# Optimization experiments

Measured on AMD Instinct MI355X. Metric: run time of the kernel, lower is better.

## Reference

```python
import jax, jax.numpy as jnp
import numpy as np

G = 1024      # graphs per batch
NPG = 64      # nodes per graph
M = 512       # undirected edges per graph (stored both directions)
N = G * NPG   # 65536 nodes
E = G * 2 * M # 1048576 directed edges
F_IN = 128
HID = 128
CLS = 10
RATIO = 0.5   # top-k edge ratio (forward arg `ratio`); eval phase (train_phase=False)


def setup_inputs() -> dict:
    rng = np.random.default_rng(0)
    # random undirected edges within each graph, i < j guaranteed
    a = rng.integers(0, NPG, (G, M))
    b = rng.integers(0, NPG - 1, (G, M))
    b = b + (b >= a)  # b != a
    i = np.minimum(a, b)
    j = np.maximum(a, b)
    off = (np.arange(G) * NPG)[:, None]
    src = (np.concatenate([i, j], axis=1) + off).reshape(-1).astype(np.int32)
    dst = (np.concatenate([j, i], axis=1) + off).reshape(-1).astype(np.int32)
    # reverse-edge pairing: within each graph block of 2M edges, fwd e <-> e+M
    rev = (np.concatenate([np.arange(M) + M, np.arange(M)])[None, :]
           + (np.arange(G) * 2 * M)[:, None]).reshape(-1).astype(np.int32)
    batch = np.repeat(np.arange(G), NPG).astype(np.int32)

    key = jax.random.key(0)
    ks = jax.random.split(key, 8)

    def lin(k, fi, fo):
        return jax.random.normal(k, (fi, fo), jnp.float32) / np.sqrt(fi).astype(np.float32)

    return dict(
        x=jax.random.normal(ks[0], (N, F_IN), jnp.float32),
        src=jnp.asarray(src), dst=jnp.asarray(dst), rev=jnp.asarray(rev),
        batch=jnp.asarray(batch),
        W0=lin(ks[1], F_IN, HID), b0=jnp.zeros((HID,), jnp.float32),
        W1=lin(ks[2], HID, HID), b1=jnp.zeros((HID,), jnp.float32),
        W2=lin(ks[3], HID, HID), b2=jnp.zeros((HID,), jnp.float32),
        lw1=lin(ks[4], HID, HID), lb1=jnp.zeros((HID,), jnp.float32),
        lw2=lin(ks[5], HID, CLS), lb2=jnp.zeros((CLS,), jnp.float32),
    )


def gcn_conv(x, W, b, src, dst, ew):
    # PyG GCNConv with self-loops (fill 1) and symmetric normalization
    h = x @ W                                      # [N,H]
    deg = jax.ops.segment_sum(ew, dst, num_segments=N) + 1.0
    dinv = jax.lax.rsqrt(deg)                      # deg >= 1 (relu'd x => ew >= 0)
    norm = dinv[src] * ew * dinv[dst]              # [E]
    agg = jax.ops.segment_sum(norm[:, None] * h[src], dst, num_segments=N)
    return agg + (dinv * dinv)[:, None] * h + b    # self-loop term + bias


def reference(x, src, dst, rev, batch, W0, b0, W1, b1, W2, b2, lw1, lb1, lw2, lb2):
    ones_e = jnp.ones((E,), x.dtype)
    x1 = jax.nn.relu(gcn_conv(x, W0, b0, src, dst, ones_e))

    # edge scores on relu'd features (nonnegative)
    scores = jnp.sum(x1[src] * x1[dst], axis=-1)   # [E]
    gid = batch[src]                               # per-edge graph id (nondecreasing)
    mask = src < dst                               # one direction per undirected edge

    # per-graph (segment) top-k over masked edges: rank within segment by score desc
    smask = jnp.where(mask, scores, -jnp.inf)
    perm = jnp.lexsort((-smask, gid))              # primary: gid, secondary: score desc
    counts = jax.ops.segment_sum(jnp.ones((E,), jnp.int32), gid, num_segments=G)
    start = jnp.cumsum(counts) - counts            # exclusive segment starts
    rank = jnp.zeros((E,), jnp.int32).at[perm].set(
        jnp.arange(E, dtype=jnp.int32) - start[gid[perm]])
    m = jax.ops.segment_sum(mask.astype(jnp.int32), gid, num_segments=G)
    k = jnp.ceil(RATIO * m.astype(jnp.float32)).astype(jnp.int32)
    sel = mask & (rank < k[gid])
    sampled = (sel | sel[rev]).astype(x.dtype)     # mirror to reverse direction

    ew = scores * sampled                          # sparse edge weights
    x2 = jax.nn.relu(gcn_conv(x1, W1, b1, src, dst, ew))
    x3 = jax.nn.relu(gcn_conv(x2, W2, b2, src, dst, ew))

    # global mean pool over nodes per graph
    nc = jax.ops.segment_sum(jnp.ones((N,), x.dtype), batch, num_segments=G)
    pooled = jax.ops.segment_sum(x3, batch, num_segments=G) / nc[:, None]

    h = jax.nn.relu(pooled @ lw1 + lb1)            # dropout is identity at eval
    logits = h @ lw2 + lb2
    return (jax.nn.log_softmax(logits, axis=-1), sampled, counts)
```

## Files before the change

kernel.cpp:

```cpp
#include <hip/hip_runtime.h>

#define G_   1024
#define NPG_ 64
#define EPG_ 1024
#define MPG_ 512
#define F_   128
#define E_   (G_*EPG_)

typedef __attribute__((ext_vector_type(8))) short bf16x8;
typedef __attribute__((ext_vector_type(4))) float f32x4;

__device__ __forceinline__ unsigned short f2bf(float f) {
    union { float f; unsigned int u; } v; v.f = f;
    unsigned int r = v.u + 0x7fffu + ((v.u >> 16) & 1u);
    return (unsigned short)(r >> 16);
}
__device__ __forceinline__ unsigned int packbf(float a, float b) {
    return (unsigned int)f2bf(a) | ((unsigned int)f2bf(b) << 16);
}

#define XASW(r, cb) ((((r) << 4) + ((cb) ^ ((r) & 15))) << 3)
#define AFSW(r, b)  ((((r) << 3) + ((b) ^ ((r) & 7))) << 3)

__global__ __launch_bounds__(256) void k_pack_w(const float* __restrict__ W0,
    const float* __restrict__ W1, const float* __restrict__ W2,
    unsigned short* __restrict__ Wp)
{
    int idx = blockIdx.x * 256 + threadIdx.x;
    int wsel = idx >> 11;
    int r = idx & 2047;
    int lane = r & 63, tc = (r >> 6) & 7, kb = r >> 9;
    const float* W = (wsel == 0) ? W0 : ((wsel == 1) ? W1 : W2);
    int col  = tc * 16 + (lane & 15);
    int row0 = kb * 32 + (lane >> 4) * 8;
    unsigned int p0 = packbf(W[(row0+0)*F_+col], W[(row0+1)*F_+col]);
    unsigned int p1 = packbf(W[(row0+2)*F_+col], W[(row0+3)*F_+col]);
    unsigned int p2 = packbf(W[(row0+4)*F_+col], W[(row0+5)*F_+col]);
    unsigned int p3 = packbf(W[(row0+6)*F_+col], W[(row0+7)*F_+col]);
    *(uint4*)(Wp + (size_t)wsel * 16384 + (size_t)r * 8) = make_uint4(p0,p1,p2,p3);
}

__global__ __launch_bounds__(256, 4) void k_fused(
    const float* __restrict__ x, const int* __restrict__ src, const int* __restrict__ dst,
    const unsigned short* __restrict__ Wp,
    const float* __restrict__ b0, const float* __restrict__ b1, const float* __restrict__ b2,
    const float* __restrict__ lw1, const float* __restrict__ lb1,
    const float* __restrict__ lw2, const float* __restrict__ lb2,
    float* __restrict__ out_log, float* __restrict__ out_sampled,
    float* __restrict__ out_counts)
{
    const int g = blockIdx.x, t = threadIdx.x;
    const int l = t & 63, w = t >> 6;
    const int q = l >> 4, cl = l & 15;
    const int base_e = g * EPG_, base_n = g * NPG_;

    __shared__ alignas(16) unsigned short XA[8192];
    __shared__ alignas(16) float buf1[4224];
    __shared__ alignas(16) float sc[MPG_];
    __shared__ unsigned char sl[EPG_], dl[EPG_];
    __shared__ int hist_i[256];
    __shared__ unsigned long long mlist[96];
    __shared__ int wsum[4];
    __shared__ float redzf[8];
    __shared__ int ideg[NPG_];
    __shared__ float dinv[NPG_];
    __shared__ int mcnt, bstar, Rrem;

    float* mtmp = (float*)hist_i;
    unsigned int*   a1p = (unsigned int*)buf1;
    unsigned short* af1 = (unsigned short*)buf1 + 4224;
    unsigned short* af2 = (unsigned short*)buf1;

    const float4* xsrc = (const float4*)(x + (size_t)base_n * F_);
    for (int i = t; i < 2048; i += 256) {
        int v = i >> 5, c4 = i & 31;
        float4 xv = xsrc[i];
        int si = XASW(v, c4 >> 1) + (c4 & 1) * 4;
        unsigned int* d2 = (unsigned int*)&XA[si];
        d2[0] = packbf(xv.x, xv.y);
        d2[1] = packbf(xv.z, xv.w);
    }
    for (int i = t; i < 2112; i += 256) a1p[i] = 0u;
    if (t < NPG_) ideg[t] = 0;
    __syncthreads();

    for (int e = t; e < EPG_; e += 256) {
        int s = src[base_e + e] - base_n;
        int d = dst[base_e + e] - base_n;
        sl[e] = (unsigned char)s; dl[e] = (unsigned char)d;
        atomicAdd(&ideg[d], 1);
        atomicAdd(&a1p[d * 33 + (s >> 1)], 1u << ((s & 1) * 16));
    }
    __syncthreads();
    if (t < NPG_) dinv[t] = rsqrtf((float)(ideg[t] + 1));
    __syncthreads();
    for (int i = t; i < 4096; i += 256) {
        int v = i >> 6, s = i & 63;
        unsigned int m = (a1p[v * 33 + (s >> 1)] >> ((s & 1) * 16)) & 0xFFFFu;
        float a = dinv[v] * dinv[s] * (float)m;
        if (v == s) a += dinv[v] * dinv[v];
        af1[AFSW(v, s >> 3) + (s & 7)] = f2bf(a);
    }
    __syncthreads();

    auto conv = [&](const unsigned short* WpX, const unsigned short* AFp,
                    const float* bias, int writeXA) {
        f32x4 cA[4][2];
        #pragma unroll
        for (int rb = 0; rb < 4; rb++) { cA[rb][0] = (f32x4)0.0f; cA[rb][1] = (f32x4)0.0f; }
        #pragma unroll
        for (int kb = 0; kb < 4; kb++) {
            bf16x8 a[4];
            #pragma unroll
            for (int rb = 0; rb < 4; rb++)
                a[rb] = *(const bf16x8*)&XA[XASW(rb*16 + cl, kb*4 + q)];
            #pragma unroll
            for (int tcw = 0; tcw < 2; tcw++) {
                int tc = 2*w + tcw;
                bf16x8 b = *(const bf16x8*)&WpX[((kb*8 + tc)*64 + l)*8];
                #pragma unroll
                for (int rb = 0; rb < 4; rb++)
                    cA[rb][tcw] = __builtin_amdgcn_mfma_f32_16x16x32_bf16(
                                      a[rb], b, cA[rb][tcw], 0, 0, 0);
            }
        }
        __syncthreads();
        #pragma unroll
        for (int rb = 0; rb < 4; rb++)
            #pragma unroll
            for (int tcw = 0; tcw < 2; tcw++) {
                int tc = 2*w + tcw;
                #pragma unroll
                for (int rp = 0; rp < 2; rp++) {
                    int r0 = rb*16 + q*4 + rp*2;
                    int idx = ((r0 >> 5)*8 + tc)*512 + (((r0 >> 3) & 3)*16 + cl)*8 + (r0 & 7);
                    *(unsigned int*)&XA[idx] = packbf(cA[rb][tcw][rp*2], cA[rb][tcw][rp*2+1]);
                }
            }
        __syncthreads();
        f32x4 cB[4][2];
        #pragma unroll
        for (int rb = 0; rb < 4; rb++) { cB[rb][0] = (f32x4)0.0f; cB[rb][1] = (f32x4)0.0f; }
        #pragma unroll
        for (int kb2 = 0; kb2 < 2; kb2++) {
            bf16x8 a2[4];
            #pragma unroll
            for (int rb = 0; rb < 4; rb++)
                a2[rb] = *(const bf16x8*)&AFp[AFSW(rb*16 + cl, kb2*4 + q)];
            #pragma unroll
            for (int tcw = 0; tcw < 2; tcw++) {
                int tc = 2*w + tcw;
                bf16x8 b2 = *(const bf16x8*)&XA[((kb2*8 + tc)*64 + l)*8];
                #pragma unroll
                for (int rb = 0; rb < 4; rb++)
                    cB[rb][tcw] = __builtin_amdgcn_mfma_f32_16x16x32_bf16(
                                      a2[rb], b2, cB[rb][tcw], 0, 0, 0);
            }
        }
        __syncthreads();
        #pragma unroll
        for (int tcw = 0; tcw < 2; tcw++) {
            int colb = (2*w + tcw)*16 + cl;
            float bv = bias[colb];
            if (writeXA) {
                #pragma unroll
                for (int rb = 0; rb < 4; rb++)
                    #pragma unroll
                    for (int reg = 0; reg < 4; reg++) {
                        int row = rb*16 + q*4 + reg;
                        XA[XASW(row, colb >> 3) + (colb & 7)] =
                            f2bf(fmaxf(cB[rb][tcw][reg] + bv, 0.0f));
                    }
            } else {
                float ps = 0.0f;
                #pragma unroll
                for (int rb = 0; rb < 4; rb++)
                    #pragma unroll
                    for (int reg = 0; reg < 4; reg++)
                        ps += fmaxf(cB[rb][tcw][reg] + bv, 0.0f);
                atomicAdd(&sc[colb], ps);
            }
        }
    };

    conv(Wp, af1, b0, 1);
    __syncthreads();

    {
        f32x4 cg[4];
        #pragma unroll
        for (int tcg = 0; tcg < 4; tcg++) cg[tcg] = (f32x4)0.0f;
        #pragma unroll
        for (int kb = 0; kb < 4; kb++) {
            bf16x8 a = *(const bf16x8*)&XA[XASW(w*16 + cl, kb*4 + q)];
            #pragma unroll
            for (int tcg = 0; tcg < 4; tcg++) {
                bf16x8 b = *(const bf16x8*)&XA[XASW(tcg*16 + cl, kb*4 + q)];
                cg[tcg] = __builtin_amdgcn_mfma_f32_16x16x32_bf16(a, b, cg[tcg], 0, 0, 0);
            }
        }
        #pragma unroll
        for (int tcg = 0; tcg < 4; tcg++)
            #pragma unroll
            for (int reg = 0; reg < 4; reg++)
                buf1[(w*16 + q*4 + reg)*66 + tcg*16 + cl] = cg[tcg][reg];
    }
    __syncthreads();

    float sA, sB;
    {
        sA = buf1[(int)sl[t]*66 + dl[t]];
        sB = buf1[(int)sl[t+256]*66 + dl[t+256]];
        sc[t] = sA; sc[t + 256] = sB;
    }
    if (t < NPG_) dinv[t] = 1.0f;
    __syncthreads();

    int selA, selB;
    {
        float mn = fminf(sA, sB), mx = fmaxf(sA, sB);
        #pragma unroll
        for (int off = 32; off >= 1; off >>= 1) {
            mn = fminf(mn, __shfl_xor(mn, off, 64));
            mx = fmaxf(mx, __shfl_xor(mx, off, 64));
        }
        if (l == 0) { redzf[w] = mn; redzf[4 + w] = mx; }
        hist_i[t] = 0;
        if (t == 0) mcnt = 0;
        __syncthreads();
        mn = fminf(fminf(redzf[0], redzf[1]), fminf(redzf[2], redzf[3]));
        mx = fmaxf(fmaxf(redzf[4], redzf[5]), fmaxf(redzf[6], redzf[7]));
        float scale = 255.0f / fmaxf(mx - mn, 1e-20f);
        int binA = (int)fminf((sA - mn) * scale, 255.0f);
        int binB = (int)fminf((sB - mn) * scale, 255.0f);
        atomicAdd(&hist_i[binA], 1);
        atomicAdd(&hist_i[binB], 1);
        __syncthreads();
        int h = hist_i[t];
        int v = h;
        #pragma unroll
        for (int off = 1; off < 64; off <<= 1) {
            int n = __shfl_down(v, off, 64);
            if (l + off < 64) v += n;
        }
        if (l == 0) wsum[w] = v;
        __syncthreads();
        int suf = v;
        for (int w2 = w + 1; w2 < 4; w2++) suf += wsum[w2];
        int cgt = suf - h;
        if (suf >= 256 && cgt < 256) { bstar = t; Rrem = 256 - cgt; }
        __syncthreads();
        const int bs = bstar, Rr = Rrem;
        unsigned long long keyA = ((unsigned long long)__float_as_uint(sA) << 32)
                                | (unsigned int)(0xFFFFFFFFu - (unsigned)t);
        unsigned long long keyB = ((unsigned long long)__float_as_uint(sB) << 32)
                                | (unsigned int)(0xFFFFFFFFu - (unsigned)(t + 256));
        if (binA == bs) { int p = atomicAdd(&mcnt, 1); if (p < 96) mlist[p] = keyA; }
        if (binB == bs) { int p = atomicAdd(&mcnt, 1); if (p < 96) mlist[p] = keyB; }
        __syncthreads();
        const int mc = mcnt;
        auto sel_edge = [&](float s, int e, int bin, unsigned long long key) -> int {
            if (bin > bs) return 1;
            if (bin < bs) return 0;
            if (mc <= 96) {
                int r = 0;
                for (int j2 = 0; j2 < mc; j2++) r += (mlist[j2] > key) ? 1 : 0;
                return r < Rr;
            }
            int r = 0;
            for (int ep = 0; ep < MPG_; ep++) {
                float sp = sc[ep];
                r += (sp > s || (sp == s && ep < e)) ? 1 : 0;
            }
            return r < 256;
        };
        selA = sel_edge(sA, t, binA, keyA);
        selB = sel_edge(sB, t + 256, binB, keyB);
        float sfA = selA ? 1.0f : 0.0f, sfB = selB ? 1.0f : 0.0f;
        out_sampled[base_e + t] = sfA;
        out_sampled[base_e + MPG_ + t] = sfA;
        out_sampled[base_e + t + 256] = sfB;
        out_sampled[base_e + MPG_ + t + 256] = sfB;
    }
    for (int i = t; i < 4224; i += 256) buf1[i] = 0.0f;
    __syncthreads();
    if (selA) {
        atomicAdd(&dinv[dl[t]], sA); atomicAdd(&dinv[sl[t]], sA);
        atomicAdd(&buf1[(int)dl[t]*66 + sl[t]], sA);
        atomicAdd(&buf1[(int)sl[t]*66 + dl[t]], sA);
    }
    if (selB) {
        atomicAdd(&dinv[dl[t+256]], sB); atomicAdd(&dinv[sl[t+256]], sB);
        atomicAdd(&buf1[(int)dl[t+256]*66 + sl[t+256]], sB);
        atomicAdd(&buf1[(int)sl[t+256]*66 + dl[t+256]], sB);
    }
    __syncthreads();
    if (t < NPG_) dinv[t] = rsqrtf(dinv[t]);
    __syncthreads();
    {
        float st[4];
        #pragma unroll
        for (int k2 = 0; k2 < 4; k2++) {
            int i = k2*256 + t; int vv = i >> 6, ss = i & 63;
            float a = dinv[vv] * dinv[ss] * buf1[vv*66 + ss];
            if (vv == ss) a += dinv[vv] * dinv[vv];
            st[k2] = a;
        }
        __syncthreads();
        #pragma unroll
        for (int k2 = 0; k2 < 4; k2++) {
            int i = k2*256 + t; int vv = i >> 6, ss = i & 63;
            af2[AFSW(vv, ss >> 3) + (ss & 7)] = f2bf(st[k2]);
        }
        for (int i = 1024 + t; i < 4096; i += 256) {
            int vv = i >> 6, ss = i & 63;
            float a = dinv[vv] * dinv[ss] * buf1[vv*66 + ss];
            if (vv == ss) a += dinv[vv] * dinv[vv];
            af2[AFSW(vv, ss >> 3) + (ss & 7)] = f2bf(a);
        }
    }
    __syncthreads();

    conv(Wp + 16384, af2, b1, 1);
    __syncthreads();

    if (t < F_) sc[t] = 0.0f;
    conv(Wp + 32768, af2, b2, 0);
    __syncthreads();

    {
        int c = t & 127, hh = t >> 7;
        float p = 0.0f;
        for (int kk = 0; kk < 64; kk++) {
            int k2 = hh*64 + kk;
            p = fmaf(sc[k2], lw1[(size_t)k2 * F_ + c], p);
        }
        mtmp[t] = p;
    }
    __syncthreads();
    if (t >= 128 && t < 138) buf1[200 + (t - 128)] = 0.0f;
    if (t < F_)
        buf1[t] = fmaxf(lb1[t] + (mtmp[t] + mtmp[t + 128]) * (1.0f/64.0f), 0.0f);
    __syncthreads();
    if (t < 160) {
        int o = t >> 4, seg = t & 15;
        float p = 0.0f;
        #pragma unroll
        for (int kk = 0; kk < 8; kk++) {
            int k2 = seg*8 + kk;
            p = fmaf(buf1[k2], lw2[(size_t)k2 * 10 + o], p);
        }
        atomicAdd(&buf1[200 + o], p);
    }
    __syncthreads();
    if (t < 10) {
        float lg = buf1[200 + t] + lb2[t];
        float m = -1e30f;
        #pragma unroll
        for (int q2 = 0; q2 < 10; q2++) m = fmaxf(m, buf1[200 + q2] + lb2[q2]);
        float se = 0.0f;
        #pragma unroll
        for (int q2 = 0; q2 < 10; q2++) se += expf(buf1[200 + q2] + lb2[q2] - m);
        out_log[(size_t)g * 10 + t] = lg - m - logf(se);
    }
    if (t == 0) out_counts[g] = 1024.0f;
}

extern "C" void kernel_launch(void* const* d_in, const int* in_sizes, int n_in,
                              void* d_out, int out_size, void* d_ws, size_t ws_size,
                              hipStream_t stream) {
    const float* x    = (const float*)d_in[0];
    const int*   src  = (const int*)  d_in[1];
    const int*   dst  = (const int*)  d_in[2];
    const float* W0   = (const float*)d_in[5];
    const float* b0   = (const float*)d_in[6];
    const float* W1   = (const float*)d_in[7];
    const float* b1   = (const float*)d_in[8];
    const float* W2   = (const float*)d_in[9];
    const float* b2   = (const float*)d_in[10];
    const float* lw1  = (const float*)d_in[11];
    const float* lb1  = (const float*)d_in[12];
    const float* lw2  = (const float*)d_in[13];
    const float* lb2  = (const float*)d_in[14];

    float* out_log     = (float*)d_out;
    float* out_sampled = out_log + (size_t)G_ * 10;
    float* out_counts  = out_sampled + (size_t)E_;

    unsigned short* Wp = (unsigned short*)d_ws;

    k_pack_w<<<24, 256, 0, stream>>>(W0, W1, W2, Wp);
    k_fused<<<G_, 256, 0, stream>>>(x, src, dst, Wp, b0, b1, b2,
                                    lw1, lb1, lw2, lb2,
                                    out_log, out_sampled, out_counts);
}
```

Baseline: 48.45 us.

## Preload weights into registers and overlap conv stages with graph preprocessing

Splits the conv lambda into separate stages. Weight fragments are now loaded into registers ahead of use, and the first X·W MFMA overlaps construction of the normalized adjacency. The second layer's X·W GEMM is fused into the gram-score MFMA loop because it reads the same activations, and several barriers are removed by moving the buffer clears and the sc reset earlier. Edge loading is also vectorised to int4 per thread. The cost is higher register pressure (three sets of eight bf16x8 weight fragments plus accumulators), which could lower occupancy or cause spills.

```diff
diff --git a/kernel.cpp b/kernel.cpp
--- a/kernel.cpp
+++ b/kernel.cpp
@@ -71,6 +71,81 @@
     unsigned short* af1 = (unsigned short*)buf1 + 4224;
     unsigned short* af2 = (unsigned short*)buf1;
 
+    auto loadW = [&](const unsigned short* WpX, bf16x8 (&wr)[8]) {
+        #pragma unroll
+        for (int kb = 0; kb < 4; kb++)
+            #pragma unroll
+            for (int tcw = 0; tcw < 2; tcw++)
+                wr[kb*2+tcw] = *(const bf16x8*)&WpX[((kb*8 + 2*w+tcw)*64 + l)*8];
+    };
+    auto mfma_step1 = [&](const bf16x8 (&wr)[8], f32x4 (&cX)[4][2]) {
+        #pragma unroll
+        for (int rb = 0; rb < 4; rb++) { cX[rb][0] = (f32x4)0.0f; cX[rb][1] = (f32x4)0.0f; }
+        #pragma unroll
+        for (int kb = 0; kb < 4; kb++) {
+            bf16x8 a[4];
+            #pragma unroll
+            for (int rb = 0; rb < 4; rb++)
+                a[rb] = *(const bf16x8*)&XA[XASW(rb*16 + cl, kb*4 + q)];
+            #pragma unroll
+            for (int tcw = 0; tcw < 2; tcw++)
+                #pragma unroll
+                for (int rb = 0; rb < 4; rb++)
+                    cX[rb][tcw] = __builtin_amdgcn_mfma_f32_16x16x32_bf16(
+                                      a[rb], wr[kb*2+tcw], cX[rb][tcw], 0, 0, 0);
+        }
+    };
+    auto write_xw = [&](const f32x4 (&cX)[4][2]) {
+        #pragma unroll
+        for (int rb = 0; rb < 4; rb++)
+            #pragma unroll
+            for (int tcw = 0; tcw < 2; tcw++) {
+                int tc = 2*w + tcw;
+                #pragma unroll
+                for (int rp = 0; rp < 2; rp++) {
+                    int r0 = rb*16 + q*4 + rp*2;
+                    int idx = ((r0 >> 5)*8 + tc)*512 + (((r0 >> 3) & 3)*16 + cl)*8 + (r0 & 7);
+                    *(unsigned int*)&XA[idx] = packbf(cX[rb][tcw][rp*2], cX[rb][tcw][rp*2+1]);
+                }
+            }
+    };
+    auto mfma_step2 = [&](const unsigned short* AFp, f32x4 (&cX)[4][2]) {
+        #pragma unroll
+        for (int rb = 0; rb < 4; rb++) { cX[rb][0] = (f32x4)0.0f; cX[rb][1] = (f32x4)0.0f; }
+        #pragma unroll
+        for (int kb2 = 0; kb2 < 2; kb2++) {
+            bf16x8 a2[4];
+            #pragma unroll
+            for (int rb = 0; rb < 4; rb++)
+                a2[rb] = *(const bf16x8*)&AFp[AFSW(rb*16 + cl, kb2*4 + q)];
+            #pragma unroll
+            for (int tcw = 0; tcw < 2; tcw++) {
+                bf16x8 b2 = *(const bf16x8*)&XA[((kb2*8 + 2*w+tcw)*64 + l)*8];
+                #pragma unroll
+                for (int rb = 0; rb < 4; rb++)
+                    cX[rb][tcw] = __builtin_amdgcn_mfma_f32_16x16x32_bf16(
+                                      a2[rb], b2, cX[rb][tcw], 0, 0, 0);
+            }
+        }
+    };
+    auto epilogue_H = [&](const f32x4 (&cX)[4][2], const float* bias) {
+        #pragma unroll
+        for (int tcw = 0; tcw < 2; tcw++) {
+            int colb = (2*w + tcw)*16 + cl;
+            float bv = bias[colb];
+            #pragma unroll
+            for (int rb = 0; rb < 4; rb++)
+                #pragma unroll
+                for (int reg = 0; reg < 4; reg++) {
+                    int row = rb*16 + q*4 + reg;
+                    XA[XASW(row, colb >> 3) + (colb & 7)] =
+                        f2bf(fmaxf(cX[rb][tcw][reg] + bv, 0.0f));
+                }
+        }
+    };
+
+    bf16x8 wr1[8];
+    loadW(Wp, wr1);
     const float4* xsrc = (const float4*)(x + (size_t)base_n * F_);
     for (int i = t; i < 2048; i += 256) {
         int v = i >> 5, c4 = i & 31;
@@ -84,120 +159,74 @@
     if (t < NPG_) ideg[t] = 0;
     __syncthreads();
 
-    for (int e = t; e < EPG_; e += 256) {
-        int s = src[base_e + e] - base_n;
-        int d = dst[base_e + e] - base_n;
-        sl[e] = (unsigned char)s; dl[e] = (unsigned char)d;
-        atomicAdd(&ideg[d], 1);
-        atomicAdd(&a1p[d * 33 + (s >> 1)], 1u << ((s & 1) * 16));
+    {
+        int4 s4 = ((const int4*)(src + base_e))[t];
+        int4 d4 = ((const int4*)(dst + base_e))[t];
+        int s0 = s4.x - base_n, s1 = s4.y - base_n, s2 = s4.z - base_n, s3 = s4.w - base_n;
+        int d0 = d4.x - base_n, d1 = d4.y - base_n, d2 = d4.z - base_n, d3 = d4.w - base_n;
+        *(uchar4*)&sl[t*4] = make_uchar4((unsigned char)s0, (unsigned char)s1,
+                                         (unsigned char)s2, (unsigned char)s3);
+        *(uchar4*)&dl[t*4] = make_uchar4((unsigned char)d0, (unsigned char)d1,
+                                         (unsigned char)d2, (unsigned char)d3);
+        atomicAdd(&ideg[d0], 1); atomicAdd(&ideg[d1], 1);
+        atomicAdd(&ideg[d2], 1); atomicAdd(&ideg[d3], 1);
+        atomicAdd(&a1p[d0 * 33 + (s0 >> 1)], 1u << ((s0 & 1) * 16));
+        atomicAdd(&a1p[d1 * 33 + (s1 >> 1)], 1u << ((s1 & 1) * 16));
+        atomicAdd(&a1p[d2 * 33 + (s2 >> 1)], 1u << ((s2 & 1) * 16));
+        atomicAdd(&a1p[d3 * 33 + (s3 >> 1)], 1u << ((s3 & 1) * 16));
     }
     __syncthreads();
     if (t < NPG_) dinv[t] = rsqrtf((float)(ideg[t] + 1));
     __syncthreads();
-    for (int i = t; i < 4096; i += 256) {
-        int v = i >> 6, s = i & 63;
-        unsigned int m = (a1p[v * 33 + (s >> 1)] >> ((s & 1) * 16)) & 0xFFFFu;
-        float a = dinv[v] * dinv[s] * (float)m;
-        if (v == s) a += dinv[v] * dinv[v];
-        af1[AFSW(v, s >> 3) + (s & 7)] = f2bf(a);
-    }
-    __syncthreads();
-
-    auto conv = [&](const unsigned short* WpX, const unsigned short* AFp,
-                    const float* bias, int writeXA) {
+
+    {
         f32x4 cA[4][2];
-        #pragma unroll
-        for (int rb = 0; rb < 4; rb++) { cA[rb][0] = (f32x4)0.0f; cA[rb][1] = (f32x4)0.0f; }
+        mfma_step1(wr1, cA);
+        for (int i = t; i < 4096; i += 256) {
+            int v = i >> 6, s = i & 63;
+            unsigned int m = (a1p[v * 33 + (s >> 1)] >> ((s & 1) * 16)) & 0xFFFFu;
+            float a = dinv[v] * dinv[s] * (float)m;
+            if (v == s) a += dinv[v] * dinv[v];
+            af1[AFSW(v, s >> 3) + (s & 7)] = f2bf(a);
+        }
+        __syncthreads();
+        write_xw(cA);
+    }
+    __syncthreads();
+
+    bf16x8 wr2[8];
+    loadW(Wp + 16384, wr2);
+    {
+        f32x4 cB[4][2];
+        mfma_step2(af1, cB);
+        __syncthreads();
+        epilogue_H(cB, b0);
+    }
+    __syncthreads();
+
+    f32x4 cC[4][2];
+    {
+        f32x4 cg[4];
+        #pragma unroll
+        for (int tcg = 0; tcg < 4; tcg++) cg[tcg] = (f32x4)0.0f;
+        #pragma unroll
+        for (int rb = 0; rb < 4; rb++) { cC[rb][0] = (f32x4)0.0f; cC[rb][1] = (f32x4)0.0f; }
         #pragma unroll
         for (int kb = 0; kb < 4; kb++) {
-            bf16x8 a[4];
+            bf16x8 a_g = *(const bf16x8*)&XA[XASW(w*16 + cl, kb*4 + q)];
+            bf16x8 a2[4];
             #pragma unroll
             for (int rb = 0; rb < 4; rb++)
-                a[rb] = *(const bf16x8*)&XA[XASW(rb*16 + cl, kb*4 + q)];
-            #pragma unroll
-            for (int tcw = 0; tcw < 2; tcw++) {
-                int tc = 2*w + tcw;
-                bf16x8 b = *(const bf16x8*)&WpX[((kb*8 + tc)*64 + l)*8];
+                a2[rb] = *(const bf16x8*)&XA[XASW(rb*16 + cl, kb*4 + q)];
+            #pragma unroll
+            for (int tcg = 0; tcg < 4; tcg++)
+                cg[tcg] = __builtin_amdgcn_mfma_f32_16x16x32_bf16(a_g, a2[tcg], cg[tcg], 0, 0, 0);
+            #pragma unroll
+            for (int tcw = 0; tcw < 2; tcw++)
                 #pragma unroll
                 for (int rb = 0; rb < 4; rb++)
-                    cA[rb][tcw] = __builtin_amdgcn_mfma_f32_16x16x32_bf16(
-                                      a[rb], b, cA[rb][tcw], 0, 0, 0);
-            }
-        }
-        __syncthreads();
-        #pragma unroll
-        for (int rb = 0; rb < 4; rb++)
-            #pragma unroll
-            for (int tcw = 0; tcw < 2; tcw++) {
-                int tc = 2*w + tcw;
-                #pragma unroll
-                for (int rp = 0; rp < 2; rp++) {
-                    int r0 = rb*16 + q*4 + rp*2;
-                    int idx = ((r0 >> 5)*8 + tc)*512 + (((r0 >> 3) & 3)*16 + cl)*8 + (r0 & 7);
-                    *(unsigned int*)&XA[idx] = packbf(cA[rb][tcw][rp*2], cA[rb][tcw][rp*2+1]);
-                }
-            }
-        __syncthreads();
-        f32x4 cB[4][2];
-        #pragma unroll
-        for (int rb = 0; rb < 4; rb++) { cB[rb][0] = (f32x4)0.0f; cB[rb][1] = (f32x4)0.0f; }
-        #pragma unroll
-        for (int kb2 = 0; kb2 < 2; kb2++) {
-            bf16x8 a2[4];
-            #pragma unroll
-            for (int rb = 0; rb < 4; rb++)
-                a2[rb] = *(const bf16x8*)&AFp[AFSW(rb*16 + cl, kb2*4 + q)];
-            #pragma unroll
-            for (int tcw = 0; tcw < 2; tcw++) {
-                int tc = 2*w + tcw;
-                bf16x8 b2 = *(const bf16x8*)&XA[((kb2*8 + tc)*64 + l)*8];
-                #pragma unroll
-                for (int rb = 0; rb < 4; rb++)
-                    cB[rb][tcw] = __builtin_amdgcn_mfma_f32_16x16x32_bf16(
-                                      a2[rb], b2, cB[rb][tcw], 0, 0, 0);
-            }
-        }
-        __syncthreads();
-        #pragma unroll
-        for (int tcw = 0; tcw < 2; tcw++) {
-            int colb = (2*w + tcw)*16 + cl;
-            float bv = bias[colb];
-            if (writeXA) {
-                #pragma unroll
-                for (int rb = 0; rb < 4; rb++)
-                    #pragma unroll
-                    for (int reg = 0; reg < 4; reg++) {
-                        int row = rb*16 + q*4 + reg;
-                        XA[XASW(row, colb >> 3) + (colb & 7)] =
-                            f2bf(fmaxf(cB[rb][tcw][reg] + bv, 0.0f));
-                    }
-            } else {
-                float ps = 0.0f;
-                #pragma unroll
-                for (int rb = 0; rb < 4; rb++)
-                    #pragma unroll
-                    for (int reg = 0; reg < 4; reg++)
-                        ps += fmaxf(cB[rb][tcw][reg] + bv, 0.0f);
-                atomicAdd(&sc[colb], ps);
-            }
-        }
-    };
-
-    conv(Wp, af1, b0, 1);
-    __syncthreads();
-
-    {
-        f32x4 cg[4];
-        #pragma unroll
-        for (int tcg = 0; tcg < 4; tcg++) cg[tcg] = (f32x4)0.0f;
-        #pragma unroll
-        for (int kb = 0; kb < 4; kb++) {
-            bf16x8 a = *(const bf16x8*)&XA[XASW(w*16 + cl, kb*4 + q)];
-            #pragma unroll
-            for (int tcg = 0; tcg < 4; tcg++) {
-                bf16x8 b = *(const bf16x8*)&XA[XASW(tcg*16 + cl, kb*4 + q)];
-                cg[tcg] = __builtin_amdgcn_mfma_f32_16x16x32_bf16(a, b, cg[tcg], 0, 0, 0);
-            }
+                    cC[rb][tcw] = __builtin_amdgcn_mfma_f32_16x16x32_bf16(
+                                      a2[rb], wr2[kb*2+tcw], cC[rb][tcw], 0, 0, 0);
         }
         #pragma unroll
         for (int tcg = 0; tcg < 4; tcg++)
@@ -208,15 +237,11 @@
     __syncthreads();
 
     float sA, sB;
-    {
-        sA = buf1[(int)sl[t]*66 + dl[t]];
-        sB = buf1[(int)sl[t+256]*66 + dl[t+256]];
-        sc[t] = sA; sc[t + 256] = sB;
-    }
+    write_xw(cC);
+    sA = buf1[(int)sl[t]*66 + dl[t]];
+    sB = buf1[(int)sl[t+256]*66 + dl[t+256]];
+    sc[t] = sA; sc[t + 256] = sB;
     if (t < NPG_) dinv[t] = 1.0f;
-    __syncthreads();
-
-    int selA, selB;
     {
         float mn = fminf(sA, sB), mx = fmaxf(sA, sB);
         #pragma unroll
@@ -225,16 +250,21 @@
             mx = fmaxf(mx, __shfl_xor(mx, off, 64));
         }
         if (l == 0) { redzf[w] = mn; redzf[4 + w] = mx; }
-        hist_i[t] = 0;
-        if (t == 0) mcnt = 0;
-        __syncthreads();
-        mn = fminf(fminf(redzf[0], redzf[1]), fminf(redzf[2], redzf[3]));
-        mx = fmaxf(fmaxf(redzf[4], redzf[5]), fmaxf(redzf[6], redzf[7]));
+    }
+    hist_i[t] = 0;
+    if (t == 0) mcnt = 0;
+    __syncthreads();
+
+    int selA, selB;
+    {
+        float mn = fminf(fminf(redzf[0], redzf[1]), fminf(redzf[2], redzf[3]));
+        float mx = fmaxf(fmaxf(redzf[4], redzf[5]), fmaxf(redzf[6], redzf[7]));
         float scale = 255.0f / fmaxf(mx - mn, 1e-20f);
         int binA = (int)fminf((sA - mn) * scale, 255.0f);
         int binB = (int)fminf((sB - mn) * scale, 255.0f);
         atomicAdd(&hist_i[binA], 1);
         atomicAdd(&hist_i[binB], 1);
+        for (int i = t; i < 4224; i += 256) buf1[i] = 0.0f;
         __syncthreads();
         int h = hist_i[t];
         int v = h;
@@ -282,8 +312,6 @@
         out_sampled[base_e + t + 256] = sfB;
         out_sampled[base_e + MPG_ + t + 256] = sfB;
     }
-    for (int i = t; i < 4224; i += 256) buf1[i] = 0.0f;
-    __syncthreads();
     if (selA) {
         atomicAdd(&dinv[dl[t]], sA); atomicAdd(&dinv[sl[t]], sA);
         atomicAdd(&buf1[(int)dl[t]*66 + sl[t]], sA);
@@ -296,6 +324,7 @@
     }
     __syncthreads();
     if (t < NPG_) dinv[t] = rsqrtf(dinv[t]);
+    if (t < F_)  sc[t] = 0.0f;
     __syncthreads();
     {
         float st[4];
@@ -321,11 +350,38 @@
     }
     __syncthreads();
 
-    conv(Wp + 16384, af2, b1, 1);
-    __syncthreads();
-
-    if (t < F_) sc[t] = 0.0f;
-    conv(Wp + 32768, af2, b2, 0);
+    bf16x8 wr3[8];
+    loadW(Wp + 32768, wr3);
+    {
+        f32x4 cB[4][2];
+        mfma_step2(af2, cB);
+        __syncthreads();
+        epilogue_H(cB, b1);
+    }
+    __syncthreads();
+
+    {
+        f32x4 cA[4][2];
+        mfma_step1(wr3, cA);
+        __syncthreads();
+        write_xw(cA);
+        __syncthreads();
+        f32x4 cB[4][2];
+        mfma_step2(af2, cB);
+        __syncthreads();
+        #pragma unroll
+        for (int tcw = 0; tcw < 2; tcw++) {
+            int colb = (2*w + tcw)*16 + cl;
+            float bv = b2[colb];
+            float ps = 0.0f;
+            #pragma unroll
+            for (int rb = 0; rb < 4; rb++)
+                #pragma unroll
+                for (int reg = 0; reg < 4; reg++)
+                    ps += fmaxf(cB[rb][tcw][reg] + bv, 0.0f);
+            atomicAdd(&sc[colb], ps);
+        }
+    }
     __syncthreads();
 
     {
```

After: 53.86 us. 1.11x slower.
